# Kernel tuning notes

Hardware: AMD Instinct MI355X
Metric: run time of the kernel (lower is better)

Reference implementation:

```python
import math
import jax, jax.numpy as jnp
import numpy as np

D_MODEL = 1024
D_INNER = 2048   # expand=2
D_STATE = 16
D_CONV = 4
DT_RANK = 64     # ceil(d_model/16)
N_LAYER = 8
INPUT_DIM = 256
BATCH = 16
TT = 64
S_IN = 13
EPS = 1e-5


def setup_inputs() -> dict:
    key = jax.random.key(0)
    ks = jax.random.split(key, 10)
    def nrm(k, shape, s):
        return jax.random.normal(k, shape, dtype=jnp.float32) * jnp.float32(s)
    a_row = jnp.log(jnp.arange(1, D_STATE + 1, dtype=jnp.float32))
    return {
        "x": jax.random.normal(ks[0], (BATCH * TT, S_IN, INPUT_DIM), dtype=jnp.float32),
        "tt": TT,
        "w_in": nrm(ks[1], (D_MODEL, INPUT_DIM), 1.0 / np.sqrt(INPUT_DIM)),
        "b_in": jnp.zeros((D_MODEL,), jnp.float32),
        "cls": nrm(ks[2], (1, 1, D_MODEL), 1.0),
        "norm_w": jnp.ones((N_LAYER, D_MODEL), jnp.float32),
        "in_proj_w": nrm(ks[3], (N_LAYER, 2 * D_INNER, D_MODEL), 1.0 / np.sqrt(D_MODEL)),
        "conv_w": nrm(ks[4], (N_LAYER, D_INNER, D_CONV), 0.3),
        "conv_b": jnp.zeros((N_LAYER, D_INNER), jnp.float32),
        "x_proj_w": nrm(ks[5], (N_LAYER, DT_RANK + 2 * D_STATE, D_INNER), 1.0 / np.sqrt(D_INNER)),
        "dt_proj_w": nrm(ks[6], (N_LAYER, D_INNER, DT_RANK), 1.0 / np.sqrt(DT_RANK)),
        "dt_proj_b": jnp.float32(-4.0) + nrm(ks[7], (N_LAYER, D_INNER), 0.1),
        "A_log": jnp.tile(a_row, (N_LAYER, D_INNER, 1)),
        "D_param": jnp.ones((N_LAYER, D_INNER), jnp.float32),
        "out_proj_w": nrm(ks[8], (N_LAYER, D_MODEL, D_INNER), 1.0 / np.sqrt(D_INNER)),
        "normf_w": jnp.ones((D_MODEL,), jnp.float32),
    }


def _rmsnorm(u, w):
    return u * jax.lax.rsqrt(jnp.mean(u * u, axis=-1, keepdims=True) + EPS) * w


def _mamba_mixer(u, ipw, cw, cb, xpw, dtw, dtb, Alog, Dp, opw):
    # u: (b, L, d_model)
    b, L, _ = u.shape
    xz = u @ ipw.T                              # (b, L, 2*di)
    di = xz.shape[-1] // 2
    xm, z = xz[..., :di], xz[..., di:]
    # causal depthwise conv1d, kernel D_CONV, truncated to L (torch padding=K-1 then [:L])
    K = cw.shape[-1]
    xp = jnp.pad(xm, ((0, 0), (K - 1, 0), (0, 0)))
    xc = cb
    for k in range(K):
        xc = xc + cw[:, k] * xp[:, k:k + L, :]
    xc = jax.nn.silu(xc)                        # (b, L, di)
    proj = xc @ xpw.T                           # (b, L, dt_rank + 2*ds)
    ds = Alog.shape[-1]
    dtr = proj.shape[-1] - 2 * ds
    dt = jax.nn.softplus(proj[..., :dtr] @ dtw.T + dtb)   # (b, L, di)
    Bm = proj[..., dtr:dtr + ds]                # (b, L, ds)
    Cm = proj[..., dtr + ds:]                   # (b, L, ds)
    A = -jnp.exp(Alog)                          # (di, ds)

    def step(hst, ins):
        dt_t, B_t, C_t, u_t = ins               # (b,di),(b,ds),(b,ds),(b,di)
        dA = jnp.exp(dt_t[..., None] * A)                       # (b, di, ds)
        dBu = dt_t[..., None] * B_t[:, None, :] * u_t[..., None]
        hst = dA * hst + dBu
        y_t = jnp.einsum('bds,bs->bd', hst, C_t)
        return hst, y_t

    h0 = jnp.zeros((b, di, ds), u.dtype)
    _, ys = jax.lax.scan(step, h0, (dt.transpose(1, 0, 2), Bm.transpose(1, 0, 2),
                                    Cm.transpose(1, 0, 2), xc.transpose(1, 0, 2)))
    y = ys.transpose(1, 0, 2) + Dp * xc
    y = y * jax.nn.silu(z)
    return y @ opw.T                            # (b, L, d_model)


def _forward(x, tt, w_in, b_in, cls, norm_w, in_proj_w, conv_w, conv_b,
             x_proj_w, dt_proj_w, dt_proj_b, A_log, D_param, out_proj_w, normf_w):
    BF, Sin, _ = x.shape
    b = BF // tt
    d = w_in.shape[0]
    h = x @ w_in.T + b_in                       # (BF, Sin, d)
    h = h.reshape(b, tt, Sin, d)
    # use_aux_tokens=False -> reward+reset and action tokens are zeros
    cls_tok = jnp.broadcast_to(cls, (b, tt, 1, d))
    z_tok = jnp.zeros((b, tt, 1, d), h.dtype)
    tokens = jnp.concatenate([cls_tok, h, z_tok, z_tok], axis=2)   # (b, tt, S, d)
    S = Sin + 3
    # sinusoidal positional encoding over tt steps, shared across S tokens of a step
    pos = jnp.arange(tt, dtype=jnp.float32)
    div = jnp.exp(jnp.arange(0, d, 2, dtype=jnp.float32) * jnp.float32(-math.log(10000.0) / d))
    ang = pos[:, None] * div[None, :]
    pe = jnp.stack([jnp.sin(ang), jnp.cos(ang)], axis=-1).reshape(tt, d)
    seq = (tokens + pe[None, :, None, :]).reshape(b, tt * S, d)

    def layer_fn(carry, p):
        hs, res = carry
        nw, ipw, cw, cb, xpw, dtw, dtb, Alog, Dp, opw = p
        res = hs + res                           # residual add (res starts at 0 == None branch)
        hn = _rmsnorm(res, nw)
        hs = _mamba_mixer(hn, ipw, cw, cb, xpw, dtw, dtb, Alog, Dp, opw)
        return (hs, res), None

    params = (norm_w, in_proj_w, conv_w, conv_b, x_proj_w,
              dt_proj_w, dt_proj_b, A_log, D_param, out_proj_w)
    (hs, res), _ = jax.lax.scan(layer_fn, (seq, jnp.zeros_like(seq)), params)
    hidden = _rmsnorm(hs + res, normf_w)         # dropout p=0 is identity
    hidden = hidden.reshape(b, tt, S, d)
    pooled = hidden[:, :, 0, :]                  # pool='cls', tt != 1
    return pooled.reshape(b * tt, d)


def reference(x, tt, w_in, b_in, cls, norm_w, in_proj_w, conv_w, conv_b,
              x_proj_w, dt_proj_w, dt_proj_b, A_log, D_param, out_proj_w, normf_w):
    return _forward(x, tt, w_in, b_in, cls, norm_w, in_proj_w, conv_w, conv_b,
                    x_proj_w, dt_proj_w, dt_proj_b, A_log, D_param, out_proj_w, normf_w)
```

## Files before the change

### kernel.cpp

```cpp
#include <hip/hip_runtime.h>
#include <hip/hip_bf16.h>
#include <math.h>

#define D_MODEL 1024
#define D_INNER 2048
#define D_STATE 16
#define D_CONV 4
#define DT_RANK 64
#define N_LAYER 8
#define INPUT_DIM 256
#define BATCH 16
#define TT 64
#define S_IN 13
#define SEQ_S 16
#define L_SEQ 1024
#define XZ_LD (2 * D_INNER)
#define PROJ_N 96
#define EPS 1e-5f

typedef __attribute__((ext_vector_type(8))) short short8;
typedef __attribute__((ext_vector_type(4))) float f32x4;

__device__ __forceinline__ unsigned short f2bu(float x) {
  unsigned int u = __float_as_uint(x);
  unsigned int r = (u + 0x7fffu + ((u >> 16) & 1u)) >> 16;
  return (unsigned short)r;
}
__device__ __forceinline__ float bu2f(unsigned short u) {
  return __uint_as_float((unsigned int)u << 16);
}

__device__ __forceinline__ void gload_lds16(const void* g, void* l) {
  __builtin_amdgcn_global_load_lds(
      (const __attribute__((address_space(1))) void*)g,
      (__attribute__((address_space(3))) void*)l, 16, 0, 0);
}

__global__ __launch_bounds__(256) void gemm_mfma(
    const unsigned short* __restrict__ A, int lda,
    const unsigned short* __restrict__ W, int ldw,
    const float* __restrict__ bias,
    float* __restrict__ C, int ldc, size_t cPartStride, int accum,
    unsigned short* __restrict__ Cb, int ldcb,
    int M, int N, int kLen, int act)
{
  __shared__ unsigned short As[128 * 32];
  __shared__ unsigned short Ws[128 * 32];
  const int tid  = threadIdx.x;
  const int wave = tid >> 6;
  const int lane = tid & 63;
  const int m0 = blockIdx.x * 128;
  const int n0 = blockIdx.y * 128;
  const int wm = (wave & 1) * 64;
  const int wn = (wave >> 1) * 64;
  const int kStart = blockIdx.z * kLen;
  if (C) C += (size_t)blockIdx.z * cPartStride;

  const int srow = (lane >> 2);
  const int scol = (lane & 3) * 8;

  f32x4 acc[4][4] = {};

  for (int k0 = kStart; k0 < kStart + kLen; k0 += 32) {
#pragma unroll
    for (int i = 0; i < 2; ++i) {
      int rowA = m0 + wave * 32 + i * 16 + srow;
      if (rowA > M - 1) rowA = M - 1;
      gload_lds16(A + (size_t)rowA * lda + k0 + scol,
                  &As[(wave * 32 + i * 16) * 32]);
      int rowW = n0 + wave * 32 + i * 16 + srow;
      if (rowW > N - 1) rowW = N - 1;
      gload_lds16(W + (size_t)rowW * ldw + k0 + scol,
                  &Ws[(wave * 32 + i * 16) * 32]);
    }
    __syncthreads();

    short8 af[4], bf[4];
#pragma unroll
    for (int mi = 0; mi < 4; ++mi)
      af[mi] = *(const short8*)&As[(wm + mi * 16 + (lane & 15)) * 32 + (lane >> 4) * 8];
#pragma unroll
    for (int ni = 0; ni < 4; ++ni)
      bf[ni] = *(const short8*)&Ws[(wn + ni * 16 + (lane & 15)) * 32 + (lane >> 4) * 8];
#pragma unroll
    for (int mi = 0; mi < 4; ++mi)
#pragma unroll
      for (int ni = 0; ni < 4; ++ni)
        acc[mi][ni] = __builtin_amdgcn_mfma_f32_16x16x32_bf16(
            af[mi], bf[ni], acc[mi][ni], 0, 0, 0);
    __syncthreads();
  }

#pragma unroll
  for (int mi = 0; mi < 4; ++mi) {
#pragma unroll
    for (int ni = 0; ni < 4; ++ni) {
      const int col = n0 + wn + ni * 16 + (lane & 15);
      if (col >= N) continue;
#pragma unroll
      for (int r = 0; r < 4; ++r) {
        const int row = m0 + wm + mi * 16 + (lane >> 4) * 4 + r;
        if (row >= M) continue;
        float v = acc[mi][ni][r];
        if (bias) v += bias[col];
        if (act == 1) v = (v > 20.f) ? v : log1pf(__expf(v));
        if (C) {
          float o = v;
          if (accum) o += C[(size_t)row * ldc + col];
          C[(size_t)row * ldc + col] = o;
        }
        if (Cb) Cb[(size_t)row * ldcb + col] = f2bu(v);
      }
    }
  }
}

__global__ __launch_bounds__(256) void xproj_combine(
    const float* __restrict__ part, float* __restrict__ proj,
    unsigned short* __restrict__ projb, int n4, size_t stride4)
{
  int i = blockIdx.x * 256 + threadIdx.x;
  if (i >= n4) return;
  float4 a = ((const float4*)part)[i];
  float4 b = ((const float4*)part)[i + stride4];
  float4 c = ((const float4*)part)[i + 2 * stride4];
  float4 d = ((const float4*)part)[i + 3 * stride4];
  float4 v = make_float4(a.x + b.x + c.x + d.x, a.y + b.y + c.y + d.y,
                         a.z + b.z + c.z + d.z, a.w + b.w + c.w + d.w);
  ((float4*)proj)[i] = v;
  ushort4 o;
  o.x = f2bu(v.x); o.y = f2bu(v.y); o.z = f2bu(v.z); o.w = f2bu(v.w);
  ((ushort4*)projb)[i] = o;
}

__global__ __launch_bounds__(256) void cvt_bf16(
    const float* __restrict__ in, unsigned short* __restrict__ out, int n4)
{
  int i = blockIdx.x * 256 + threadIdx.x;
  if (i < n4) {
    float4 v = ((const float4*)in)[i];
    ushort4 o;
    o.x = f2bu(v.x); o.y = f2bu(v.y); o.z = f2bu(v.z); o.w = f2bu(v.w);
    ((ushort4*)out)[i] = o;
  }
}

__device__ __forceinline__ float block_reduce_sum_256(float v)
{
  __shared__ float red[4];
#pragma unroll
  for (int off = 32; off > 0; off >>= 1) v += __shfl_xor(v, off, 64);
  const int tid = threadIdx.x;
  if ((tid & 63) == 0) red[tid >> 6] = v;
  __syncthreads();
  return red[0] + red[1] + red[2] + red[3];
}

__global__ __launch_bounds__(256) void seq_build(
    const float* __restrict__ hflat, const float* __restrict__ cls,
    float* __restrict__ res)
{
  const int row = blockIdx.x;
  const int bl = row >> 10;
  const int l = row & (L_SEQ - 1);
  const int t = l >> 4;
  const int s = l & 15;
  const int tid = threadIdx.x;

  float4 v;
  if (s == 0) {
    v = ((const float4*)cls)[tid];
  } else if (s <= S_IN) {
    const size_t hrow = ((size_t)(bl * TT + t) * S_IN + (s - 1)) * D_MODEL;
    v = ((const float4*)(hflat + hrow))[tid];
  } else {
    v = make_float4(0.f, 0.f, 0.f, 0.f);
  }

  const float cexp = -logf(10000.f) / (float)D_MODEL;
  float pe[4];
#pragma unroll
  for (int j = 0; j < 4; ++j) {
    int d = tid * 4 + j;
    int i2 = d & ~1;
    float ang = (float)t * expf((float)i2 * cexp);
    pe[j] = (d & 1) ? cosf(ang) : sinf(ang);
  }
  v.x += pe[0]; v.y += pe[1]; v.z += pe[2]; v.w += pe[3];

  ((float4*)(res + (size_t)row * D_MODEL))[tid] = v;
}

__global__ __launch_bounds__(256) void rmsnorm_only(
    const float* __restrict__ res, unsigned short* __restrict__ hnb,
    const float* __restrict__ w)
{
  const int row = blockIdx.x;
  const int tid = threadIdx.x;
  const size_t base = (size_t)row * D_MODEL;
  float4 r = ((const float4*)(res + base))[tid];
  float ss = r.x * r.x + r.y * r.y + r.z * r.z + r.w * r.w;
  ss = block_reduce_sum_256(ss);
  const float scale = rsqrtf(ss * (1.f / (float)D_MODEL) + EPS);
  float4 wv = ((const float4*)w)[tid];
  ushort4 o;
  o.x = f2bu(r.x * scale * wv.x);
  o.y = f2bu(r.y * scale * wv.y);
  o.z = f2bu(r.z * scale * wv.z);
  o.w = f2bu(r.w * scale * wv.w);
  ((ushort4*)(hnb + base))[tid] = o;
}

__global__ __launch_bounds__(256) void conv_silu(
    const unsigned short* __restrict__ xzb, const float* __restrict__ cw,
    const float* __restrict__ cb, unsigned short* __restrict__ xcb)
{
  const int c = (blockIdx.x * 256 + threadIdx.x) * 4;
  const int t = blockIdx.y;
  const int bl = blockIdx.z;
  const unsigned row = (unsigned)bl * L_SEQ + t;

  float4 w0 = *(const float4*)&cw[(c + 0) * D_CONV];
  float4 w1 = *(const float4*)&cw[(c + 1) * D_CONV];
  float4 w2 = *(const float4*)&cw[(c + 2) * D_CONV];
  float4 w3 = *(const float4*)&cw[(c + 3) * D_CONV];
  float4 bias = *(const float4*)&cb[c];
  float a0 = bias.x, a1 = bias.y, a2 = bias.z, a3 = bias.w;

#define CONV_TAP(k, wk)                                                      \
  if (t >= 3 - (k)) {                                                        \
    ushort4 xv = *(const ushort4*)&xzb[(size_t)(row - 3 + (k)) * XZ_LD + c]; \
    a0 = fmaf(w0.wk, bu2f(xv.x), a0);                                        \
    a1 = fmaf(w1.wk, bu2f(xv.y), a1);                                        \
    a2 = fmaf(w2.wk, bu2f(xv.z), a2);                                        \
    a3 = fmaf(w3.wk, bu2f(xv.w), a3);                                        \
  }
  CONV_TAP(0, x)
  CONV_TAP(1, y)
  CONV_TAP(2, z)
  CONV_TAP(3, w)
#undef CONV_TAP

  a0 = a0 / (1.f + __expf(-a0));
  a1 = a1 / (1.f + __expf(-a1));
  a2 = a2 / (1.f + __expf(-a2));
  a3 = a3 / (1.f + __expf(-a3));
  ushort4 o;
  o.x = f2bu(a0); o.y = f2bu(a1); o.z = f2bu(a2); o.w = f2bu(a3);
  *(ushort4*)&xcb[(size_t)row * D_INNER + c] = o;
}

__global__ __launch_bounds__(256) void scan7(
    const unsigned short* __restrict__ xzb,
    const unsigned short* __restrict__ xzbz,
    unsigned short* xcb,
    const float* __restrict__ proj,
    const float* __restrict__ Alog, const float* __restrict__ Dp)
{
  const int tid  = threadIdx.x;
  const int lane = tid & 63;
  const int wave = tid >> 6;
  const int chl  = lane >> 2;
  const int sq   = lane & 3;
  const int ch   = blockIdx.x * 64 + wave * 16 + chl;
  const int s0   = sq * 4;
  const int bl   = blockIdx.y;

  float A2[4], h[4] = {0.f, 0.f, 0.f, 0.f};
#pragma unroll
  for (int k = 0; k < 4; ++k)
    A2[k] = -__expf(Alog[(size_t)ch * D_STATE + s0 + k]) * 1.44269504f;
  const float Dv = Dp[ch];

  unsigned odt = ((unsigned)bl * (L_SEQ * XZ_LD) + (unsigned)ch) * 2u;
  unsigned ou  = ((unsigned)bl * (L_SEQ * D_INNER) + (unsigned)ch) * 2u;
  unsigned oB  = ((unsigned)bl * (L_SEQ * PROJ_N) + (unsigned)(DT_RANK + s0)) * 4u;
  unsigned ost = ou;

  float pdt[4], pz[4], pu[4];
  float4 pB[4], pC[4];

#define SCAN_LOAD(slot)                                                       \
  {                                                                           \
    pdt[slot] = bu2f(*(const unsigned short*)((const char*)xzb + odt));       \
    pz[slot]  = bu2f(*(const unsigned short*)((const char*)xzbz + odt));      \
    pu[slot]  = bu2f(*(const unsigned short*)((const char*)xcb + ou));        \
    pB[slot]  = *(const float4*)((const char*)proj + oB);                     \
    pC[slot]  = *(const float4*)((const char*)proj + oB + D_STATE * 4);       \
    odt += XZ_LD * 2; ou += D_INNER * 2; oB += PROJ_N * 4;                    \
  }

  SCAN_LOAD(0)
  SCAN_LOAD(1)
  SCAN_LOAD(2)

#pragma unroll 4
  for (int t = 0; t < L_SEQ; ++t) {
    const int sl = t & 3;
    SCAN_LOAD((t + 3) & 3)

    const float dtv = pdt[sl];
    const float u   = pu[sl];
    const float du  = dtv * u;
    const float4 B4 = pB[sl];
    const float4 C4 = pC[sl];
    const float Bk[4] = {B4.x, B4.y, B4.z, B4.w};
    const float Ck[4] = {C4.x, C4.y, C4.z, C4.w};
    float yv = 0.f;
#pragma unroll
    for (int k = 0; k < 4; ++k) {
      const float dA = exp2f(dtv * A2[k]);
      h[k] = fmaf(dA, h[k], du * Bk[k]);
      yv = fmaf(h[k], Ck[k], yv);
    }
    yv += __shfl_xor(yv, 1, 64);
    yv += __shfl_xor(yv, 2, 64);
    if (sq == 0) {
      const float zv = pz[sl];
      const float g = zv / (1.f + __expf(-zv));
      *(unsigned short*)((char*)xcb + ost) = f2bu(fmaf(Dv, u, yv) * g);
    }
    ost += D_INNER * 2;
  }
#undef SCAN_LOAD
}

__global__ __launch_bounds__(256) void pool_norm(
    const float* __restrict__ res, const float* __restrict__ w,
    float* __restrict__ out, int b0)
{
  const int idx = blockIdx.x;
  const int bl = idx >> 6;
  const int t = idx & 63;
  const size_t base = ((size_t)bl * L_SEQ + (size_t)t * SEQ_S) * D_MODEL;
  const int tid = threadIdx.x;
  float4 v = ((const float4*)(res + base))[tid];
  float ss = v.x * v.x + v.y * v.y + v.z * v.z + v.w * v.w;
  ss = block_reduce_sum_256(ss);
  const float scale = rsqrtf(ss * (1.f / (float)D_MODEL) + EPS);
  float4 wv = ((const float4*)w)[tid];
  float4 o = make_float4(v.x * scale * wv.x, v.y * scale * wv.y,
                         v.z * scale * wv.z, v.w * scale * wv.w);
  const size_t orow = (size_t)((b0 + bl) * TT + t) * D_MODEL;
  ((float4*)(out + orow))[tid] = o;
}

extern "C" void kernel_launch(void* const* d_in, const int* in_sizes, int n_in,
                              void* d_out, int out_size, void* d_ws, size_t ws_size,
                              hipStream_t stream)
{
  const float* x      = (const float*)d_in[0];
  const float* w_in   = (const float*)d_in[2];
  const float* b_in   = (const float*)d_in[3];
  const float* cls    = (const float*)d_in[4];
  const float* norm_w = (const float*)d_in[5];
  const float* ipw    = (const float*)d_in[6];
  const float* cw     = (const float*)d_in[7];
  const float* cb     = (const float*)d_in[8];
  const float* xpw    = (const float*)d_in[9];
  const float* dtw    = (const float*)d_in[10];
  const float* dtb    = (const float*)d_in[11];
  const float* Alog   = (const float*)d_in[12];
  const float* Dp     = (const float*)d_in[13];
  const float* opw    = (const float*)d_in[14];
  const float* normfw = (const float*)d_in[15];
  float* out = (float*)d_out;

  const size_t N_WIN = (size_t)D_MODEL * INPUT_DIM;
  const size_t N_IPW = (size_t)N_LAYER * XZ_LD * D_MODEL;
  const size_t N_XPW = (size_t)N_LAYER * PROJ_N * D_INNER;
  const size_t N_DTW = (size_t)N_LAYER * D_INNER * DT_RANK;
  const size_t N_OPW = (size_t)N_LAYER * D_MODEL * D_INNER;
  const size_t N_XB  = (size_t)BATCH * TT * S_IN * INPUT_DIM;
  const size_t N_BF  = N_WIN + N_IPW + N_XPW + N_DTW + N_OPW + N_XB;

  const size_t perB = (size_t)L_SEQ * 19008;
  int bc = 0;
  for (int c = 16; c >= 1; c >>= 1)
    if (N_BF * 2 + perB * (size_t)c <= ws_size) { bc = c; break; }
  if (bc == 0) return;

  const int R = bc * L_SEQ;

  unsigned short* w_in_b = (unsigned short*)d_ws;
  unsigned short* ipw_b  = w_in_b + N_WIN;
  unsigned short* xpw_b  = ipw_b + N_IPW;
  unsigned short* dtw_b  = xpw_b + N_XPW;
  unsigned short* opw_b  = dtw_b + N_DTW;
  unsigned short* x_b    = opw_b + N_OPW;
  float*          res  = (float*)(x_b + N_XB);
  unsigned short* xzb  = (unsigned short*)(res + (size_t)R * D_MODEL);
  unsigned short* xcb  = xzb + (size_t)R * XZ_LD;
  float*          proj = (float*)(xcb + (size_t)R * D_INNER);
  unsigned short* projb = (unsigned short*)(proj + (size_t)R * PROJ_N);
  unsigned short* hnb   = projb + (size_t)R * PROJ_N;
  float* ppart = (float*)hnb;
  float* hflat = (float*)xzb;

  cvt_bf16<<<(int)((N_WIN/4 + 255)/256), 256, 0, stream>>>(w_in, w_in_b, (int)(N_WIN/4));
  cvt_bf16<<<(int)((N_IPW/4 + 255)/256), 256, 0, stream>>>(ipw, ipw_b, (int)(N_IPW/4));
  cvt_bf16<<<(int)((N_XPW/4 + 255)/256), 256, 0, stream>>>(xpw, xpw_b, (int)(N_XPW/4));
  cvt_bf16<<<(int)((N_DTW/4 + 255)/256), 256, 0, stream>>>(dtw, dtw_b, (int)(N_DTW/4));
  cvt_bf16<<<(int)((N_OPW/4 + 255)/256), 256, 0, stream>>>(opw, opw_b, (int)(N_OPW/4));
  cvt_bf16<<<(int)((N_XB/4  + 255)/256), 256, 0, stream>>>(x,   x_b,   (int)(N_XB/4));

  for (int b0 = 0; b0 < BATCH; b0 += bc) {
    const int Mx = bc * TT * S_IN;
    gemm_mfma<<<dim3((Mx + 127) / 128, D_MODEL / 128), 256, 0, stream>>>(
        x_b + (size_t)b0 * TT * S_IN * INPUT_DIM, INPUT_DIM,
        w_in_b, INPUT_DIM, b_in, hflat, D_MODEL, 0, 0, nullptr, 0,
        Mx, D_MODEL, INPUT_DIM, 0);

    seq_build<<<R, 256, 0, stream>>>(hflat, cls, res);

    for (int l = 0; l < N_LAYER; ++l) {
      rmsnorm_only<<<R, 256, 0, stream>>>(res, hnb,
          norm_w + (size_t)l * D_MODEL);

      gemm_mfma<<<dim3(R / 128, XZ_LD / 128), 256, 0, stream>>>(
          hnb, D_MODEL, ipw_b + (size_t)l * XZ_LD * D_MODEL, D_MODEL,
          nullptr, nullptr, 0, 0, 0, xzb, XZ_LD, R, XZ_LD, D_MODEL, 0);

      conv_silu<<<dim3(D_INNER / 1024, L_SEQ, bc), 256, 0, stream>>>(
          xzb, cw + (size_t)l * D_INNER * D_CONV, cb + (size_t)l * D_INNER,
          xcb);

      gemm_mfma<<<dim3(R / 128, 1, 4), 256, 0, stream>>>(
          xcb, D_INNER, xpw_b + (size_t)l * PROJ_N * D_INNER, D_INNER,
          nullptr, ppart, PROJ_N, (size_t)R * PROJ_N, 0, nullptr, 0,
          R, PROJ_N, 512, 0);
      xproj_combine<<<(R * PROJ_N / 4 + 255) / 256, 256, 0, stream>>>(
          ppart, proj, projb, R * PROJ_N / 4, (size_t)R * PROJ_N / 4);

      gemm_mfma<<<dim3(R / 128, D_INNER / 128), 256, 0, stream>>>(
          projb, PROJ_N, dtw_b + (size_t)l * D_INNER * DT_RANK, DT_RANK,
          dtb + (size_t)l * D_INNER, nullptr, 0, 0, 0, xzb, XZ_LD,
          R, D_INNER, 64, 1);

      scan7<<<dim3(D_INNER / 64, bc), 256, 0, stream>>>(
          xzb, xzb + D_INNER, xcb, proj,
          Alog + (size_t)l * D_INNER * D_STATE, Dp + (size_t)l * D_INNER);

      gemm_mfma<<<dim3(R / 128, D_MODEL / 128), 256, 0, stream>>>(
          xcb, D_INNER, opw_b + (size_t)l * D_MODEL * D_INNER, D_INNER,
          nullptr, res, D_MODEL, 0, 1, nullptr, 0, R, D_MODEL, D_INNER, 0);
    }

    pool_norm<<<bc * TT, 256, 0, stream>>>(res, normfw, out, b0);
  }
}
```

Measured before the change: 8.423 ms.

## Assign one channel per thread with all 16 states in registers in scan

The selective scan now gives each thread one channel and all 16 SSM states, instead of four lanes per channel with four states each. This removes the per-step cross-lane shuffle reduction and the lane-0-only store. B and C are read as wave-uniform broadcast loads with double buffering. In exchange the grid has 4x fewer threads (64-thread blocks, one wave per block), which lowers latency hiding, and each thread does 16 exp2 per step in a serial chain while using more registers.

```diff
diff --git a/kernel.cpp b/kernel.cpp
--- a/kernel.cpp
+++ b/kernel.cpp
@@ -250,79 +250,91 @@
   *(ushort4*)&xcb[(size_t)row * D_INNER + c] = o;
 }
 
-__global__ __launch_bounds__(256) void scan7(
+__global__ __launch_bounds__(64) void scan8(
     const unsigned short* __restrict__ xzb,
     const unsigned short* __restrict__ xzbz,
     unsigned short* xcb,
     const float* __restrict__ proj,
     const float* __restrict__ Alog, const float* __restrict__ Dp)
 {
-  const int tid  = threadIdx.x;
-  const int lane = tid & 63;
-  const int wave = tid >> 6;
-  const int chl  = lane >> 2;
-  const int sq   = lane & 3;
-  const int ch   = blockIdx.x * 64 + wave * 16 + chl;
-  const int s0   = sq * 4;
-  const int bl   = blockIdx.y;
-
-  float A2[4], h[4] = {0.f, 0.f, 0.f, 0.f};
-#pragma unroll
-  for (int k = 0; k < 4; ++k)
-    A2[k] = -__expf(Alog[(size_t)ch * D_STATE + s0 + k]) * 1.44269504f;
+  const int tid = threadIdx.x;
+  const int ch  = blockIdx.x * 64 + tid;
+  const int bl  = blockIdx.y;
+
+  float A2[16], h[16];
+  {
+    const float4* ap = (const float4*)&Alog[(size_t)ch * D_STATE];
+#pragma unroll
+    for (int q = 0; q < 4; ++q) {
+      float4 a4 = ap[q];
+      A2[q*4+0] = -__expf(a4.x) * 1.44269504f;
+      A2[q*4+1] = -__expf(a4.y) * 1.44269504f;
+      A2[q*4+2] = -__expf(a4.z) * 1.44269504f;
+      A2[q*4+3] = -__expf(a4.w) * 1.44269504f;
+    }
+#pragma unroll
+    for (int k = 0; k < 16; ++k) h[k] = 0.f;
+  }
   const float Dv = Dp[ch];
 
   unsigned odt = ((unsigned)bl * (L_SEQ * XZ_LD) + (unsigned)ch) * 2u;
   unsigned ou  = ((unsigned)bl * (L_SEQ * D_INNER) + (unsigned)ch) * 2u;
-  unsigned oB  = ((unsigned)bl * (L_SEQ * PROJ_N) + (unsigned)(DT_RANK + s0)) * 4u;
   unsigned ost = ou;
 
+  const float4* pBC = (const float4*)(proj + (size_t)bl * (L_SEQ * PROJ_N)
+                                      + DT_RANK);
+
   float pdt[4], pz[4], pu[4];
-  float4 pB[4], pC[4];
-
-#define SCAN_LOAD(slot)                                                       \
+  float Bv[2][16], Cv[2][16];
+
+#define LOADU(slot)                                                           \
   {                                                                           \
     pdt[slot] = bu2f(*(const unsigned short*)((const char*)xzb + odt));       \
     pz[slot]  = bu2f(*(const unsigned short*)((const char*)xzbz + odt));      \
     pu[slot]  = bu2f(*(const unsigned short*)((const char*)xcb + ou));        \
-    pB[slot]  = *(const float4*)((const char*)proj + oB);                     \
-    pC[slot]  = *(const float4*)((const char*)proj + oB + D_STATE * 4);       \
-    odt += XZ_LD * 2; ou += D_INNER * 2; oB += PROJ_N * 4;                    \
-  }
-
-  SCAN_LOAD(0)
-  SCAN_LOAD(1)
-  SCAN_LOAD(2)
+    odt += XZ_LD * 2; ou += D_INNER * 2;                                      \
+  }
+#define LOADBC(buf)                                                           \
+  {                                                                           \
+    _Pragma("unroll")                                                         \
+    for (int q = 0; q < 4; ++q) {                                             \
+      float4 b4 = pBC[q];                                                     \
+      float4 c4 = pBC[q + 4];                                                 \
+      Bv[buf][q*4+0] = b4.x; Bv[buf][q*4+1] = b4.y;                           \
+      Bv[buf][q*4+2] = b4.z; Bv[buf][q*4+3] = b4.w;                           \
+      Cv[buf][q*4+0] = c4.x; Cv[buf][q*4+1] = c4.y;                           \
+      Cv[buf][q*4+2] = c4.z; Cv[buf][q*4+3] = c4.w;                           \
+    }                                                                         \
+    pBC += PROJ_N / 4;                                                        \
+  }
+
+  LOADU(0) LOADU(1) LOADU(2)
+  LOADBC(0)
 
 #pragma unroll 4
   for (int t = 0; t < L_SEQ; ++t) {
     const int sl = t & 3;
-    SCAN_LOAD((t + 3) & 3)
+    const int bb = t & 1;
+    LOADU((t + 3) & 3)
+    LOADBC(bb ^ 1)
 
     const float dtv = pdt[sl];
     const float u   = pu[sl];
     const float du  = dtv * u;
-    const float4 B4 = pB[sl];
-    const float4 C4 = pC[sl];
-    const float Bk[4] = {B4.x, B4.y, B4.z, B4.w};
-    const float Ck[4] = {C4.x, C4.y, C4.z, C4.w};
     float yv = 0.f;
 #pragma unroll
-    for (int k = 0; k < 4; ++k) {
+    for (int k = 0; k < 16; ++k) {
       const float dA = exp2f(dtv * A2[k]);
-      h[k] = fmaf(dA, h[k], du * Bk[k]);
-      yv = fmaf(h[k], Ck[k], yv);
+      h[k] = fmaf(dA, h[k], du * Bv[bb][k]);
+      yv = fmaf(h[k], Cv[bb][k], yv);
     }
-    yv += __shfl_xor(yv, 1, 64);
-    yv += __shfl_xor(yv, 2, 64);
-    if (sq == 0) {
-      const float zv = pz[sl];
-      const float g = zv / (1.f + __expf(-zv));
-      *(unsigned short*)((char*)xcb + ost) = f2bu(fmaf(Dv, u, yv) * g);
-    }
+    const float zv = pz[sl];
+    const float g = zv / (1.f + __expf(-zv));
+    *(unsigned short*)((char*)xcb + ost) = f2bu(fmaf(Dv, u, yv) * g);
     ost += D_INNER * 2;
   }
-#undef SCAN_LOAD
+#undef LOADU
+#undef LOADBC
 }
 
 __global__ __launch_bounds__(256) void pool_norm(
@@ -437,7 +449,7 @@
           dtb + (size_t)l * D_INNER, nullptr, 0, 0, 0, xzb, XZ_LD,
           R, D_INNER, 64, 1);
 
-      scan7<<<dim3(D_INNER / 64, bc), 256, 0, stream>>>(
+      scan8<<<dim3(D_INNER / 64, bc), 64, 0, stream>>>(
           xzb, xzb + D_INNER, xcb, proj,
           Alog + (size_t)l * D_INNER * D_STATE, Dp + (size_t)l * D_INNER);
 
```

Measured after the change: 15.13 ms. +79.7%, slower.
